# Performance work log

Measured on AMD Instinct MI355X. Metric: run time of the kernel, lower is better.

The kernel has to match this reference:

```python
import jax, jax.numpy as jnp
import numpy as np

N, C, H, W = 32, 512, 32, 32
S = 2048
INFLUENCE = 1.0  # influence_decay='constant', training_progress irrelevant


def setup_inputs() -> dict:
    key = jax.random.key(0)
    k1, k2 = jax.random.split(key)
    x = jax.random.normal(k1, (N, C, H, W), dtype=jnp.float32)
    # nn.Parameter(torch.randn(S, C) / C)
    codebook = jax.random.normal(k2, (S, C), dtype=jnp.float32) / C
    return {"x": x, "codebook": codebook}


def _distances(x_flat, codebook):
    # x_flat: [N, C, P], codebook: [S, C] -> [N, S, P]
    # same math as ((x[:,None]-cb[None,...,None])**2).sum(2), without the
    # [N, S, C, P] intermediate
    x2 = jnp.sum(x_flat * x_flat, axis=1)          # [N, P]
    c2 = jnp.sum(codebook * codebook, axis=1)      # [S]
    xc = jnp.einsum('ncp,sc->nsp', x_flat, codebook)  # [N, S, P]
    return x2[:, None, :] + c2[None, :, None] - 2.0 * xc


def reference(x, codebook):
    n, c = x.shape[:2]
    x_flat = x.reshape(n, c, -1)                      # [N, C, P]
    xs = jax.lax.stop_gradient(x_flat)                # distance(x_flat.detach())
    d = _distances(xs, codebook)                      # [N, S, P]
    idx = jnp.argmin(d, axis=1)                       # [N, P]
    xq = jnp.transpose(codebook[idx], (0, 2, 1)).reshape(x.shape)  # [N,C,H,W]
    loss_commitment = jnp.mean((x - jax.lax.stop_gradient(xq)) ** 2)
    d_sorted = jnp.sort(d, axis=1)                    # ascending over S
    w = jnp.exp(-jnp.arange(d.shape[1], dtype=jnp.float32) / INFLUENCE)
    loss_codebook = jnp.mean(w[None, :, None] * d_sorted)
    codebook_indices = idx.reshape(n, *x.shape[2:])   # [N, H, W]
    output = x + jax.lax.stop_gradient(xq - x)        # straight-through
    return (loss_codebook, loss_commitment, codebook_indices, output)
```

## Files before the change

kernel.cpp:

```cpp
#include <hip/hip_runtime.h>
#include <hip/hip_fp16.h>

#define N_ 32
#define C_ 512
#define P_ 1024
#define S_ 2048
#define NR_ (N_ * P_)
#define GUARD 6e-3f
#define TSIG 2.3f

typedef __attribute__((ext_vector_type(8))) short sh8;
typedef __attribute__((ext_vector_type(4))) float fx4;

#define WS_XT       0ull
#define WS_XTF      33554432ull
#define WS_CBT      100663296ull
#define WS_C2F      102760448ull
#define WS_X2       102768640ull
#define WS_CNT      102899712ull
#define WS_CAND     103030784ull
#define WS_ROWPART  119808000ull
#define WS_COMMIT   120070144ull
#define WS_TOTAL    120201216ull

#define TBLK 1024
#define CVTBLK 512

__device__ __forceinline__ unsigned short f2bf(float f) {
  union { float f; unsigned u; } x; x.f = f;
  unsigned r = x.u + 0x7fffu + ((x.u >> 16) & 1u);
  return (unsigned short)(r >> 16);
}

template <typename T>
__device__ __forceinline__ void load16_lds(const T* g, T* l) {
  __builtin_amdgcn_global_load_lds((const __attribute__((address_space(1))) void*)g,
                                   (__attribute__((address_space(3))) void*)l, 16, 0, 0);
}

__global__ __launch_bounds__(256) void k_prep(const float* __restrict__ x,
                                              const float* __restrict__ cb,
                                              unsigned short* __restrict__ xT,
                                              float* __restrict__ xTf,
                                              unsigned short* __restrict__ cbT,
                                              float* __restrict__ c2f,
                                              float* __restrict__ x2ws,
                                              int* __restrict__ cnt) {
  __shared__ float tile[32][260];
  const int tid = threadIdx.x;
  const int bx = blockIdx.x;

  if (bx < TBLK) {
    const int n = bx >> 5;
    const int p0 = (bx & 31) << 5;
    const float* xb = x + (size_t)n * (C_ * P_) + p0;
    const int p4 = (tid & 7) << 2;
    const int ch = tid >> 3;

    float acc = 0.f;
#pragma unroll
    for (int pass = 0; pass < 2; ++pass) {
      if (pass) __syncthreads();
#pragma unroll
      for (int it = 0; it < 8; ++it) {
        int cl = (it << 5) + ch;
        float4 v = *(const float4*)(xb + (size_t)(pass * 256 + cl) * P_ + p4);
        tile[p4 + 0][cl] = v.x;
        tile[p4 + 1][cl] = v.y;
        tile[p4 + 2][cl] = v.z;
        tile[p4 + 3][cl] = v.w;
      }
      __syncthreads();

#pragma unroll
      for (int it = 0; it < 8; ++it) {
        int idx = tid + 256 * it;
        int row = idx >> 6, c4 = (idx & 63) << 2;
        float4 f = *(const float4*)&tile[row][c4];
        size_t R = (size_t)((n << 10) + p0 + row);
        size_t cg = (size_t)pass * 256 + c4;
        *(float4*)(xTf + R * C_ + cg) = f;
        ushort4 o;
        o.x = f2bf(f.x); o.y = f2bf(f.y); o.z = f2bf(f.z); o.w = f2bf(f.w);
        *(ushort4*)(xT + R * C_ + cg) = o;
      }

      if (tid < 32) {
        for (int c = 0; c < 256; ++c) {
          float t = tile[tid][c];
          acc = __fadd_rn(acc, __fmul_rn(t, t));
        }
      }
    }
    if (tid < 32) {
      int R = (n << 10) + p0 + tid;
      x2ws[R] = acc;
      cnt[R] = 0;
    }
  } else {
    const int s = (bx - TBLK) * 4 + (tid >> 6);
    const int l = tid & 63;
    const float* row = cb + (size_t)s * C_;
    double c2d = 0.0;
#pragma unroll
    for (int h = 0; h < 2; ++h) {
      int c = h * 256 + l * 4;
      float4 v = *(const float4*)(row + c);
      ushort4 o;
      o.x = f2bf(v.x); o.y = f2bf(v.y); o.z = f2bf(v.z); o.w = f2bf(v.w);
      *(ushort4*)(cbT + (size_t)s * C_ + c) = o;
      c2d += (double)__fmul_rn(v.x, v.x) + (double)__fmul_rn(v.y, v.y) +
             (double)__fmul_rn(v.z, v.z) + (double)__fmul_rn(v.w, v.w);
    }
#pragma unroll
    for (int off = 32; off > 0; off >>= 1) c2d += __shfl_down(c2d, off);
    if (l == 0) c2f[s] = (float)c2d;
  }
}

__global__ __launch_bounds__(256, 4) void k_gemm(const unsigned short* __restrict__ xT,
                                                 const unsigned short* __restrict__ cbT,
                                                 const float* __restrict__ x2ws,
                                                 uint2* __restrict__ cand,
                                                 int* __restrict__ cnt) {
  __shared__ unsigned short As[128 * 64];
  __shared__ unsigned short Bs[128 * 64];
  __shared__ float t_lds[128];
  const int tid = threadIdx.x;
  const int w = tid >> 6, l = tid & 63;
  const int bx = blockIdx.x;
  const int m_tile = ((bx >> 7) << 3) + (bx & 7);
  const int s_tile = (bx >> 3) & 15;
  const int m0 = m_tile << 7, s0 = s_tile << 7;
  const int wm = (w & 1) << 6, wsf = (w >> 1) << 6;
  const int quad = l >> 4, lane15 = l & 15;

  if (tid < 128) t_lds[tid] = TSIG * __fsqrt_rn(x2ws[m0 + tid]) * (1.0f / 512.0f);

  size_t gA[4], gB[4];
  unsigned short *lA[4], *lB[4];
#pragma unroll
  for (int q = 0; q < 4; ++q) {
    int chunk = (q * 4 + w) * 64 + l;
    int m = chunk >> 3, k8s = chunk & 7;
    int k8 = k8s ^ (m & 7);
    gA[q] = (size_t)(m0 + m) * (C_ * 2) + (size_t)k8 * 16;
    gB[q] = (size_t)(s0 + m) * (C_ * 2) + (size_t)k8 * 16;
    lA[q] = As + (q * 4 + w) * 512;
    lB[q] = Bs + (q * 4 + w) * 512;
  }
  const char* xb = (const char*)xT;
  const char* cbb = (const char*)cbT;

  fx4 acc[4][4];
#pragma unroll
  for (int i = 0; i < 4; ++i)
#pragma unroll
    for (int j = 0; j < 4; ++j) acc[i][j] = (fx4){0.f, 0.f, 0.f, 0.f};

  for (int kk = 0; kk < 8; ++kk) {
#pragma unroll
    for (int q = 0; q < 4; ++q) {
      load16_lds((const unsigned short*)(xb + gA[q] + (size_t)kk * 128), lA[q]);
      load16_lds((const unsigned short*)(cbb + gB[q] + (size_t)kk * 128), lB[q]);
    }
    __syncthreads();
#pragma unroll
    for (int ks = 0; ks < 2; ++ks) {
      const int k8g = ks * 4 + quad;
      sh8 af[4], bf[4];
#pragma unroll
      for (int mi = 0; mi < 4; ++mi) {
        int m = wm + mi * 16 + lane15;
        af[mi] = *(const sh8*)(As + m * 64 + (k8g ^ (m & 7)) * 8);
      }
#pragma unroll
      for (int si = 0; si < 4; ++si) {
        int s = wsf + si * 16 + lane15;
        bf[si] = *(const sh8*)(Bs + s * 64 + (k8g ^ (s & 7)) * 8);
      }
#pragma unroll
      for (int mi = 0; mi < 4; ++mi)
#pragma unroll
        for (int si = 0; si < 4; ++si)
          acc[mi][si] = __builtin_amdgcn_mfma_f32_16x16x32_bf16(af[mi], bf[si], acc[mi][si], 0, 0, 0);
    }
    __syncthreads();
  }

  const unsigned below = (1u << lane15) - 1u;
#pragma unroll
  for (int mi = 0; mi < 4; ++mi) {
#pragma unroll
    for (int r = 0; r < 4; ++r) {
      const int rowl = wm + mi * 16 + quad * 4 + r;
      const int rowg = m0 + rowl;
      const float t = t_lds[rowl];
      float v[4]; int scol[4]; bool hit[4];
      float vmax = -1e30f; int smax = 0;
#pragma unroll
      for (int si = 0; si < 4; ++si) {
        v[si] = acc[mi][si][r];
        scol[si] = s0 + wsf + si * 16 + lane15;
        hit[si] = v[si] >= t;
        if (v[si] > vmax) { vmax = v[si]; smax = scol[si]; }
      }
      int total = 0, myslot[4];
#pragma unroll
      for (int si = 0; si < 4; ++si) {
        unsigned long long b = __ballot(hit[si]);
        unsigned seg = (unsigned)((b >> (quad * 16)) & 0xFFFFull);
        myslot[si] = total + __popc(seg & below);
        total += __popc(seg);
      }
#pragma unroll
      for (int off = 1; off < 16; off <<= 1) {
        float ov = __shfl_xor(vmax, off);
        int os = __shfl_xor(smax, off);
        if (ov > vmax) { vmax = ov; smax = os; }
      }
      int base = 0;
      if (lane15 == 0) base = atomicAdd(&cnt[rowg], total > 0 ? total : 1);
      base = __shfl(base, quad * 16);
      if (total > 0) {
#pragma unroll
        for (int si = 0; si < 4; ++si) {
          if (hit[si]) {
            int slot = base + myslot[si];
            if (slot < 64) {
              cand[(size_t)rowg * 64 + slot] =
                  make_uint2(__float_as_uint(v[si]), (unsigned)scol[si]);
            }
          }
        }
      } else if (lane15 == 0 && base < 64) {
        cand[(size_t)rowg * 64 + base] =
            make_uint2(__float_as_uint(vmax), (unsigned)smax);
      }
    }
  }
}

__global__ __launch_bounds__(256, 4) void k_phase2(
    const float* __restrict__ cb, const float* __restrict__ xTf,
    const uint2* __restrict__ candG,
    const int* __restrict__ cntG, const float* __restrict__ c2f,
    const float* __restrict__ x2ws, float* __restrict__ out,
    double* __restrict__ rowpart) {
  __shared__ float xrow[4][C_];
  const int tid = threadIdx.x;
  const int w = tid >> 6, l = tid & 63;
  const int R = blockIdx.x * 4 + w;

  const int cnt = min(cntG[R], 64);
  const float x2f = x2ws[R];
  const bool act = l < cnt;
  uint2 ce = candG[(size_t)R * 64 + l];
  float v = __uint_as_float(ce.x);
  int s = (int)ce.y;
  v = act ? v : -1e30f;
  s = act ? s : 0x7fffffff;
  const int sIdx = act ? s : 0;
  const float dt = act
      ? __fsub_rn(__fadd_rn(x2f, c2f[sIdx]), __fmul_rn(2.f, v))
      : 1e30f;

  float M = v;
#pragma unroll
  for (int off = 1; off < 64; off <<= 1) M = fmaxf(M, __shfl_xor(M, off));

  int rank = 0;
  for (int k = 0; k < 64; ++k) {
    float dk = __shfl(dt, k);
    int sk = __shfl(s, k);
    rank += (dk < dt || (dk == dt && sk < s)) ? 1 : 0;
  }

  double contrib = act ? (double)__expf(-(float)rank) * (double)dt : 0.0;
#pragma unroll
  for (int off = 32; off > 0; off >>= 1) contrib += __shfl_down(contrib, off);
  if (l == 0) rowpart[R] = contrib;

  const bool near = act && (v >= M - GUARD);
  const unsigned long long bal = __ballot(near);
  const int nres = __popcll(bal);
  if (nres == 1) {
    int src = __ffsll(bal) - 1;
    int wins = __shfl(s, src);
    if (l == 0) out[2 + R] = (float)wins;
  } else {
#pragma unroll
    for (int k = 0; k < 2; ++k)
      *(float4*)&xrow[w][l * 8 + k * 4] = *(const float4*)(xTf + (size_t)R * C_ + l * 8 + k * 4);
    float d32 = 1e30f;
    if (near) {
      const float4* crow = (const float4*)(cb + (size_t)s * C_);
      float acc = 0.f;
#pragma unroll 8
      for (int i = 0; i < C_ / 4; ++i) {
        float4 cv = crow[i];
        float4 xv = *(const float4*)&xrow[w][i * 4];
        acc = __fadd_rn(acc, __fmul_rn(xv.x, cv.x));
        acc = __fadd_rn(acc, __fmul_rn(xv.y, cv.y));
        acc = __fadd_rn(acc, __fmul_rn(xv.z, cv.z));
        acc = __fadd_rn(acc, __fmul_rn(xv.w, cv.w));
      }
      d32 = __fsub_rn(__fadd_rn(x2f, c2f[s]), __fmul_rn(2.f, acc));
    }
    float bd = d32;
    int bs2 = near ? s : 0x7fffffff;
#pragma unroll
    for (int off = 1; off < 64; off <<= 1) {
      float ov = __shfl_xor(bd, off);
      int os = __shfl_xor(bs2, off);
      if (ov < bd || (ov == bd && os < bs2)) { bd = ov; bs2 = os; }
    }
    if (l == 0) out[2 + R] = (float)bs2;
  }
}

__global__ __launch_bounds__(256) void k2_output(
    const float* __restrict__ x, const float* __restrict__ cb,
    float* __restrict__ out, double* __restrict__ commit_partial) {
  __shared__ float qt[16][516];
  __shared__ int s_lds[16];
  __shared__ double r2[4];
  const int tid = threadIdx.x;
  const int bx = blockIdx.x;
  const int n = bx >> 6;
  const int p0 = (bx & 63) << 4;

  if (tid < 16) s_lds[tid] = (int)out[2 + n * P_ + p0 + tid];
  __syncthreads();
  {
    const int p = tid >> 4, c0 = (tid & 15) << 2;
    const float* row = cb + (size_t)s_lds[p] * C_;
#pragma unroll
    for (int it = 0; it < 8; ++it) {
      int c = c0 + (it << 6);
      *(float4*)&qt[p][c] = *(const float4*)(row + c);
    }
  }
  __syncthreads();

  const int cl = tid >> 2, pq = (tid & 3) << 2;
  double dacc = 0.0;
#pragma unroll
  for (int chunk = 0; chunk < 8; ++chunk) {
    int c = (chunk << 6) + cl;
    const float* xr = x + ((size_t)n * C_ + c) * P_ + p0 + pq;
    float4 xv = *(const float4*)xr;
    float xs[4] = {xv.x, xv.y, xv.z, xv.w};
    float o[4];
    float acc = 0.f;
#pragma unroll
    for (int k = 0; k < 4; ++k) {
      float q = qt[pq + k][c];
      float t = __fsub_rn(q, xs[k]);
      o[k] = __fadd_rn(xs[k], t);
      float dd = __fsub_rn(xs[k], q);
      acc += dd * dd;
    }
    float* orow = out + 2 + N_ * P_ + ((size_t)n * C_ + c) * P_ + p0 + pq;
    *(float4*)orow = make_float4(o[0], o[1], o[2], o[3]);
    dacc += (double)acc;
  }

#pragma unroll
  for (int off = 32; off > 0; off >>= 1) dacc += __shfl_down(dacc, off);
  if ((tid & 63) == 0) r2[tid >> 6] = dacc;
  __syncthreads();
  if (tid == 0) commit_partial[bx] = r2[0] + r2[1] + r2[2] + r2[3];
}

__global__ __launch_bounds__(256) void k3_finalize(
    const double* __restrict__ pa, int na, const double* __restrict__ pb, int nb,
    float* __restrict__ out) {
  __shared__ double red[8];
  const int tid = threadIdx.x;
  double a = 0.0, b = 0.0;
  for (int i = tid; i < na; i += 256) a += pa[i];
  for (int i = tid; i < nb; i += 256) b += pb[i];
#pragma unroll
  for (int off = 32; off > 0; off >>= 1) {
    a += __shfl_down(a, off);
    b += __shfl_down(b, off);
  }
  if ((tid & 63) == 0) {
    red[(tid >> 6) * 2 + 0] = a;
    red[(tid >> 6) * 2 + 1] = b;
  }
  __syncthreads();
  if (tid == 0) {
    double A = red[0] + red[2] + red[4] + red[6];
    double B = red[1] + red[3] + red[5] + red[7];
    out[0] = (float)(A / ((double)N_ * (double)S_ * (double)P_));
    out[1] = (float)(B / ((double)N_ * (double)C_ * (double)P_));
  }
}

#define TPW 8
#define KC 32
#define SC 64
#define KCF 48
__global__ __launch_bounds__(256) void k1_fallback(
    const float* __restrict__ x, const float* __restrict__ cb,
    float* __restrict__ out, double* __restrict__ cb_partial) {
  __shared__ float dval[TPW][KCF];
  __shared__ float x2f[TPW];
  __shared__ double redd[4];
  __shared__ float x_t[TPW][C_ + 4];
  __shared__ float cb_t[SC][KC + 4];
  __shared__ int cand_s[TPW][KCF];
  __shared__ _Float16 sc[S_][TPW];

  const int tid = threadIdx.x;
  const int bx = blockIdx.x;
  const int n = bx >> 7;
  const int p0 = (bx & 127) * TPW;

  const float* xn = x + (size_t)n * C_ * P_ + p0;
#pragma unroll
  for (int q = 0; q < 16; ++q) {
    int e = tid + 256 * q;
    int c = e >> 3, j = e & 7;
    x_t[j][c] = xn[(size_t)c * P_ + j];
  }
  __syncthreads();
  if (tid < TPW) {
    float acc = 0.f;
    for (int c = 0; c < C_; ++c)
      acc = __fadd_rn(acc, __fmul_rn(x_t[tid][c], x_t[tid][c]));
    x2f[tid] = acc;
  }
  const int j = tid & 7;
  const int sg = tid >> 3;
  for (int s0 = 0; s0 < S_; s0 += SC) {
    float acc0 = 0.f, acc1 = 0.f;
    for (int k0 = 0; k0 < C_; k0 += KC) {
      __syncthreads();
#pragma unroll
      for (int q = 0; q < 8; ++q) {
        int e = tid + 256 * q;
        int i = e >> 5, cc = e & 31;
        cb_t[i][cc] = cb[(size_t)(s0 + i) * C_ + k0 + cc];
      }
      __syncthreads();
      const float* xr = &x_t[j][k0];
#pragma unroll
      for (int cs = 0; cs < KC; cs += 4) {
        float4 xv = *(const float4*)(xr + cs);
        float4 a4 = *(const float4*)(&cb_t[sg][cs]);
        float4 b4 = *(const float4*)(&cb_t[sg + 32][cs]);
        acc0 += xv.x * a4.x + xv.y * a4.y + xv.z * a4.z + xv.w * a4.w;
        acc1 += xv.x * b4.x + xv.y * b4.y + xv.z * b4.z + xv.w * b4.w;
      }
    }
    sc[s0 + sg][j] = (_Float16)acc0;
    sc[s0 + sg + 32][j] = (_Float16)acc1;
  }
  __syncthreads();
  {
    const int g = tid >> 5, t = tid & 31;
    for (int pass = 0; pass < KCF; ++pass) {
      float bv = -1e30f;
      int bs = 0;
      for (int k = 0; k < 64; ++k) {
        int s = t + 32 * k;
        float vv = (float)sc[s][g];
        if (vv > bv) { bv = vv; bs = s; }
      }
#pragma unroll
      for (int off = 1; off < 32; off <<= 1) {
        float ov = __shfl_xor(bv, off);
        int os = __shfl_xor(bs, off);
        if (ov > bv || (ov == bv && os < bs)) { bv = ov; bs = os; }
      }
      if (t == 0) {
        cand_s[g][pass] = bs;
        sc[bs][g] = (_Float16)(-65504.f);
      }
      __syncthreads();
    }
  }
  for (int task = tid; task < TPW * KCF; task += 256) {
    int jj = task / KCF, r = task % KCF;
    int s = cand_s[jj][r];
    const float* row = cb + (size_t)s * C_;
    const float* xrw = &x_t[jj][0];
    float acc = 0.f;
    double c2d = 0.0;
    for (int c = 0; c < C_; c += 4) {
      float4 cv = *(const float4*)(row + c);
      acc = __fadd_rn(acc, __fmul_rn(xrw[c + 0], cv.x));
      acc = __fadd_rn(acc, __fmul_rn(xrw[c + 1], cv.y));
      acc = __fadd_rn(acc, __fmul_rn(xrw[c + 2], cv.z));
      acc = __fadd_rn(acc, __fmul_rn(xrw[c + 3], cv.w));
      c2d += (double)__fmul_rn(cv.x, cv.x);
      c2d += (double)__fmul_rn(cv.y, cv.y);
      c2d += (double)__fmul_rn(cv.z, cv.z);
      c2d += (double)__fmul_rn(cv.w, cv.w);
    }
    float c2s = (float)c2d;
    dval[jj][r] = __fsub_rn(__fadd_rn(x2f[jj], c2s), __fmul_rn(2.f, acc));
  }
  __syncthreads();
  double contrib = 0.0;
  for (int task = tid; task < TPW * KCF; task += 256) {
    int jj = task / KCF, r = task % KCF;
    float e = dval[jj][r];
    int s = cand_s[jj][r];
    int rank = 0;
    for (int r2 = 0; r2 < KCF; ++r2) {
      float e2 = dval[jj][r2];
      int s2 = cand_s[jj][r2];
      rank += (e2 < e || (e2 == e && s2 < s)) ? 1 : 0;
    }
    contrib += exp((double)(-rank)) * (double)e;
    if (rank == 0) out[2 + n * P_ + p0 + jj] = (float)s;
  }
  __syncthreads();
#pragma unroll
  for (int off = 32; off > 0; off >>= 1) contrib += __shfl_down(contrib, off);
  if ((tid & 63) == 0) redd[tid >> 6] = contrib;
  __syncthreads();
  if (tid == 0) cb_partial[bx] = redd[0] + redd[1] + redd[2] + redd[3];
}

extern "C" void kernel_launch(void* const* d_in, const int* in_sizes, int n_in,
                              void* d_out, int out_size, void* d_ws, size_t ws_size,
                              hipStream_t stream) {
  const float* x = (const float*)d_in[0];
  const float* cb = (const float*)d_in[1];
  float* out = (float*)d_out;
  char* ws = (char*)d_ws;

  if (ws_size >= WS_TOTAL) {
    unsigned short* xT = (unsigned short*)(ws + WS_XT);
    float* xTf = (float*)(ws + WS_XTF);
    unsigned short* cbT = (unsigned short*)(ws + WS_CBT);
    float* c2f = (float*)(ws + WS_C2F);
    float* x2ws = (float*)(ws + WS_X2);
    int* cnt = (int*)(ws + WS_CNT);
    uint2* cand = (uint2*)(ws + WS_CAND);
    double* rowpart = (double*)(ws + WS_ROWPART);
    double* commitp = (double*)(ws + WS_COMMIT);

    hipLaunchKernelGGL(k_prep, dim3(TBLK + CVTBLK), dim3(256), 0, stream,
                       x, cb, xT, xTf, cbT, c2f, x2ws, cnt);
    hipLaunchKernelGGL(k_gemm, dim3(4096), dim3(256), 0, stream,
                       xT, cbT, x2ws, cand, cnt);
    hipLaunchKernelGGL(k_phase2, dim3(NR_ / 4), dim3(256), 0, stream,
                       cb, xTf, cand, cnt, c2f, x2ws, out, rowpart);
    hipLaunchKernelGGL(k2_output, dim3(2048), dim3(256), 0, stream, x, cb, out, commitp);
    hipLaunchKernelGGL(k3_finalize, dim3(1), dim3(256), 0, stream,
                       rowpart, NR_, commitp, 2048, out);
  } else {
    double* cb_partial = (double*)d_ws;
    double* commitp = cb_partial + 4096;
    hipLaunchKernelGGL(k1_fallback, dim3(4096), dim3(256), 0, stream, x, cb, out, cb_partial);
    hipLaunchKernelGGL(k2_output, dim3(2048), dim3(256), 0, stream, x, cb, out, commitp);
    hipLaunchKernelGGL(k3_finalize, dim3(1), dim3(256), 0, stream,
                       cb_partial, 4096, commitp, 2048, out);
  }
}
```

Baseline: 432.8 us.

## Batch candidate atomics, split candidate arrays, rank via LDS reads

In the GEMM epilogue, all 16 per-row atomicAdd calls are issued up front in a separate pass so their latencies overlap, instead of one serialized atomic per row. Candidate value and index are now stored in two separate arrays instead of interleaved uint2 pairs. Phase 2 ranks candidates by reading vectorized float4/int4 values from LDS instead of 128 cross-lane shuffles. The cost is recomputing the ballots, holding 16 extra registers, and a wave-local LDS sync that relies on an explicit waitcnt without a barrier.

```diff
diff --git a/kernel.cpp b/kernel.cpp
--- a/kernel.cpp
+++ b/kernel.cpp
@@ -18,7 +18,8 @@
 #define WS_C2F      102760448ull
 #define WS_X2       102768640ull
 #define WS_CNT      102899712ull
-#define WS_CAND     103030784ull
+#define WS_CANDV    103030784ull
+#define WS_CANDS    111419392ull
 #define WS_ROWPART  119808000ull
 #define WS_COMMIT   120070144ull
 #define WS_TOTAL    120201216ull
@@ -121,7 +122,8 @@
 __global__ __launch_bounds__(256, 4) void k_gemm(const unsigned short* __restrict__ xT,
                                                  const unsigned short* __restrict__ cbT,
                                                  const float* __restrict__ x2ws,
-                                                 uint2* __restrict__ cand,
+                                                 float* __restrict__ candv,
+                                                 int* __restrict__ cands,
                                                  int* __restrict__ cnt) {
   __shared__ unsigned short As[128 * 64];
   __shared__ unsigned short Bs[128 * 64];
@@ -188,11 +190,32 @@
     __syncthreads();
   }
 
+  int baseReg[16];
+#pragma unroll
+  for (int mi = 0; mi < 4; ++mi) {
+#pragma unroll
+    for (int r = 0; r < 4; ++r) {
+      const int it = mi * 4 + r;
+      const int rowl = wm + mi * 16 + quad * 4 + r;
+      const int rowg = m0 + rowl;
+      const float t = t_lds[rowl];
+      int total = 0;
+#pragma unroll
+      for (int si = 0; si < 4; ++si) {
+        unsigned long long b = __ballot(acc[mi][si][r] >= t);
+        total += __popc((unsigned)((b >> (quad * 16)) & 0xFFFFull));
+      }
+      baseReg[it] = 0;
+      if (lane15 == 0) baseReg[it] = atomicAdd(&cnt[rowg], total > 0 ? total : 1);
+    }
+  }
+
   const unsigned below = (1u << lane15) - 1u;
 #pragma unroll
   for (int mi = 0; mi < 4; ++mi) {
 #pragma unroll
     for (int r = 0; r < 4; ++r) {
+      const int it = mi * 4 + r;
       const int rowl = wm + mi * 16 + quad * 4 + r;
       const int rowg = m0 + rowl;
       const float t = t_lds[rowl];
@@ -219,23 +242,21 @@
         int os = __shfl_xor(smax, off);
         if (ov > vmax) { vmax = ov; smax = os; }
       }
-      int base = 0;
-      if (lane15 == 0) base = atomicAdd(&cnt[rowg], total > 0 ? total : 1);
-      base = __shfl(base, quad * 16);
+      int base = __shfl(baseReg[it], quad * 16);
       if (total > 0) {
 #pragma unroll
         for (int si = 0; si < 4; ++si) {
           if (hit[si]) {
             int slot = base + myslot[si];
             if (slot < 64) {
-              cand[(size_t)rowg * 64 + slot] =
-                  make_uint2(__float_as_uint(v[si]), (unsigned)scol[si]);
+              candv[(size_t)rowg * 64 + slot] = v[si];
+              cands[(size_t)rowg * 64 + slot] = scol[si];
             }
           }
         }
       } else if (lane15 == 0 && base < 64) {
-        cand[(size_t)rowg * 64 + base] =
-            make_uint2(__float_as_uint(vmax), (unsigned)smax);
+        candv[(size_t)rowg * 64 + base] = vmax;
+        cands[(size_t)rowg * 64 + base] = smax;
       }
     }
   }
@@ -243,11 +264,13 @@
 
 __global__ __launch_bounds__(256, 4) void k_phase2(
     const float* __restrict__ cb, const float* __restrict__ xTf,
-    const uint2* __restrict__ candG,
+    const float* __restrict__ candvG, const int* __restrict__ candsG,
     const int* __restrict__ cntG, const float* __restrict__ c2f,
     const float* __restrict__ x2ws, float* __restrict__ out,
     double* __restrict__ rowpart) {
   __shared__ float xrow[4][C_];
+  __shared__ float dt_l[4][64];
+  __shared__ int s_l[4][64];
   const int tid = threadIdx.x;
   const int w = tid >> 6, l = tid & 63;
   const int R = blockIdx.x * 4 + w;
@@ -255,9 +278,8 @@
   const int cnt = min(cntG[R], 64);
   const float x2f = x2ws[R];
   const bool act = l < cnt;
-  uint2 ce = candG[(size_t)R * 64 + l];
-  float v = __uint_as_float(ce.x);
-  int s = (int)ce.y;
+  float v = candvG[(size_t)R * 64 + l];
+  int s = candsG[(size_t)R * 64 + l];
   v = act ? v : -1e30f;
   s = act ? s : 0x7fffffff;
   const int sIdx = act ? s : 0;
@@ -269,11 +291,19 @@
 #pragma unroll
   for (int off = 1; off < 64; off <<= 1) M = fmaxf(M, __shfl_xor(M, off));
 
+  dt_l[w][l] = dt;
+  s_l[w][l] = s;
+  asm volatile("s_waitcnt lgkmcnt(0)" ::: "memory");
+
   int rank = 0;
-  for (int k = 0; k < 64; ++k) {
-    float dk = __shfl(dt, k);
-    int sk = __shfl(s, k);
-    rank += (dk < dt || (dk == dt && sk < s)) ? 1 : 0;
+#pragma unroll
+  for (int k4 = 0; k4 < 16; ++k4) {
+    float4 dk = *(const float4*)&dt_l[w][k4 * 4];
+    int4 sk = *(const int4*)&s_l[w][k4 * 4];
+    rank += (dk.x < dt || (dk.x == dt && sk.x < s)) ? 1 : 0;
+    rank += (dk.y < dt || (dk.y == dt && sk.y < s)) ? 1 : 0;
+    rank += (dk.z < dt || (dk.z == dt && sk.z < s)) ? 1 : 0;
+    rank += (dk.w < dt || (dk.w == dt && sk.w < s)) ? 1 : 0;
   }
 
   double contrib = act ? (double)__expf(-(float)rank) * (double)dt : 0.0;
@@ -542,16 +572,17 @@
     float* c2f = (float*)(ws + WS_C2F);
     float* x2ws = (float*)(ws + WS_X2);
     int* cnt = (int*)(ws + WS_CNT);
-    uint2* cand = (uint2*)(ws + WS_CAND);
+    float* candv = (float*)(ws + WS_CANDV);
+    int* cands = (int*)(ws + WS_CANDS);
     double* rowpart = (double*)(ws + WS_ROWPART);
     double* commitp = (double*)(ws + WS_COMMIT);
 
     hipLaunchKernelGGL(k_prep, dim3(TBLK + CVTBLK), dim3(256), 0, stream,
                        x, cb, xT, xTf, cbT, c2f, x2ws, cnt);
     hipLaunchKernelGGL(k_gemm, dim3(4096), dim3(256), 0, stream,
-                       xT, cbT, x2ws, cand, cnt);
+                       xT, cbT, x2ws, candv, cands, cnt);
     hipLaunchKernelGGL(k_phase2, dim3(NR_ / 4), dim3(256), 0, stream,
-                       cb, xTf, cand, cnt, c2f, x2ws, out, rowpart);
+                       cb, xTf, candv, cands, cnt, c2f, x2ws, out, rowpart);
     hipLaunchKernelGGL(k2_output, dim3(2048), dim3(256), 0, stream, x, cb, out, commitp);
     hipLaunchKernelGGL(k3_finalize, dim3(1), dim3(256), 0, stream,
                        rowpart, NR_, commitp, 2048, out);
```

New measurement: 459.0 us. +6.0%, slower.
